# Kernel optimization log

Hardware: AMD Instinct MI355X
Metric: run time of the kernel (lower is better)

Reference implementation:

```python
import jax, jax.numpy as jnp
import numpy as np

VIEWS, N, D = 6, 20000, 512
BN_EPS = 1e-5


def setup_inputs() -> dict:
    key = jax.random.key(0)
    ks = jax.random.split(key, 8)
    s = 1.0 / np.sqrt(D)
    u = lambda k, shape: jax.random.uniform(k, shape, jnp.float32, -s, s)
    return {
        "latent_feature": jax.random.normal(ks[0], (VIEWS, N, D), jnp.float32),
        "WQ_w": u(ks[1], (D, D)), "WQ_b": u(ks[2], (D,)),
        "WK_w": u(ks[3], (D, D)), "WK_b": u(ks[4], (D,)),
        "WV_w": u(ks[5], (D, D)), "WV_b": u(ks[6], (D,)),
        "g_q": jnp.ones((D,), jnp.float32), "b_q": jnp.zeros((D,), jnp.float32),
        "g_k": jnp.ones((D,), jnp.float32), "b_k": jnp.zeros((D,), jnp.float32),
        "g_v": jnp.ones((D,), jnp.float32), "b_v": jnp.zeros((D,), jnp.float32),
    }


def _batchnorm(x, gamma, beta):
    # BatchNorm1d in training mode: stats over all (view, N) samples per channel
    mean = jnp.mean(x, axis=(0, 1), keepdims=True)
    var = jnp.mean((x - mean) ** 2, axis=(0, 1), keepdims=True)  # biased var
    return gamma * (x - mean) * jax.lax.rsqrt(var + BN_EPS) + beta


def _fro_normalize(x):
    # Frobenius norm per view over (N, D)
    n = jnp.sqrt(jnp.sum(x * x, axis=(1, 2), keepdims=True)) + 1e-8
    return x / n


def _multi_projection(P):
    dim = P.shape[0]
    P = 0.5 * (jax.nn.softmax(P, axis=0) + jax.nn.softmax(P, axis=1))
    for _ in range(10):  # fixed 10-step doubly-stochastic projection
        P1 = jnp.maximum(P, 0.0)
        P2 = P1 - (jnp.sum(P1, axis=1, keepdims=True) - 1.0) / dim
        P = P2 - (jnp.sum(P2, axis=0, keepdims=True) - 1.0) / dim
    return P


def reference(latent_feature, WQ_w, WQ_b, WK_w, WK_b, WV_w, WV_b,
              g_q, b_q, g_k, b_k, g_v, b_v):
    # latent_feature: [views, N, D]
    Q = _batchnorm(latent_feature @ WQ_w.T + WQ_b, g_q, b_q)
    K = _batchnorm(latent_feature @ WK_w.T + WK_b, g_k, b_k)
    V = _batchnorm(latent_feature @ WV_w.T + WV_b, g_v, b_v)
    Q, K, V = _fro_normalize(Q), _fro_normalize(K), _fro_normalize(V)
    P = jax.nn.sigmoid(jnp.einsum('ind,jnd->ij', Q, K))  # [views, views]
    P = _multi_projection(P)
    return jnp.einsum('ij,ind->jnd', P, V)  # [views, N, D]
```

## Files before the change

kernel.cpp:

```cpp
#include <hip/hip_runtime.h>

#define VIEWS 6
#define NPTS 20000
#define DIM 512
#define M_TOTAL (VIEWS * NPTS)

typedef __bf16 bf16_t;
typedef __attribute__((ext_vector_type(8))) __bf16 bf16x8;
typedef __attribute__((ext_vector_type(4))) float f32x4;

#define OFF_XB 0L
#define OFF_QB 122880000L
#define OFF_KB 245760000L
#define OFF_VB 368640000L
#define OFF_WB 491520000L
#define OFF_F32 493092864L
#define S_SUM 0
#define S_SSQ 9216
#define S_PPRE 18432
#define S_COEFA 18468
#define S_COEFC 20004
#define S_INVN 21540
#define S_P 21558
#define S_END 21594

__device__ __forceinline__ void gload_lds16(const void* gsrc, void* lds) {
    __builtin_amdgcn_global_load_lds(
        (const __attribute__((address_space(1))) unsigned int*)gsrc,
        (__attribute__((address_space(3))) unsigned int*)lds,
        16, 0, 0);
}

__global__ __launch_bounds__(256) void convert_bf16(
    const float* __restrict__ src, bf16_t* __restrict__ dst, long n8)
{
    long i = (long)blockIdx.x * blockDim.x + threadIdx.x;
    const long stride = (long)gridDim.x * blockDim.x;
    for (; i < n8; i += stride) {
        const float4* s = (const float4*)(src + i * 8);
        float4 x = s[0], y = s[1];
        bf16x8 o;
        o[0] = (bf16_t)x.x; o[1] = (bf16_t)x.y; o[2] = (bf16_t)x.z; o[3] = (bf16_t)x.w;
        o[4] = (bf16_t)y.x; o[5] = (bf16_t)y.y; o[6] = (bf16_t)y.z; o[7] = (bf16_t)y.w;
        *(bf16x8*)(dst + i * 8) = o;
    }
}

__global__ __launch_bounds__(256, 4) void gemm_qkv_mfma(
    const bf16_t* __restrict__ XB, const bf16_t* __restrict__ WB,
    const float* __restrict__ b0, const float* __restrict__ b1,
    const float* __restrict__ b2,
    float* __restrict__ statS, float* __restrict__ statQ,
    bf16_t* __restrict__ QB, bf16_t* __restrict__ KB, bf16_t* __restrict__ VB)
{
    const int orig = blockIdx.x;
    const int L    = (orig & 7) * 1878 + (orig >> 3);
    const int n0i  = L / 48;
    const int rem  = L - n0i * 48;
    const int v    = rem >> 3;
    const int c0   = (rem & 7) << 6;
    const int n0   = n0i * 64;
    const int nvalid = min(64, NPTS - n0);

    const int tid  = threadIdx.x;
    const int wid  = tid >> 6;
    const int lane = tid & 63;
    const int lr   = lane & 15;
    const int lk   = lane >> 4;
    const int wm   = wid >> 1;
    const int wn   = wid & 1;

    __shared__ char smem[32768];

    const bf16_t* Ag = XB + ((long)v * NPTS + n0) * DIM;

    f32x4 acc[3][2][2];
    const f32x4 zero4 = {0.f, 0.f, 0.f, 0.f};
#pragma unroll
    for (int t = 0; t < 3; ++t)
#pragma unroll
        for (int i = 0; i < 2; ++i)
#pragma unroll
            for (int j = 0; j < 2; ++j) acc[t][i][j] = zero4;

    for (int k0 = 0; k0 < DIM; k0 += 64) {
        __syncthreads();
#pragma unroll
        for (int i = 0; i < 8; ++i) {
            const int base = i * 256 + wid * 64;
            const int g    = base + lane;
            const bf16_t* src;
            if (g < 512) {
                const int row = g >> 3;
                const int kcs = (g & 7) ^ (row & 7);
                const int rowc = (row < nvalid) ? row : (nvalid - 1);
                src = Ag + (long)rowc * DIM + k0 + kcs * 8;
            } else {
                const int h   = g - 512;
                const int t   = h >> 9;
                const int idx = h & 511;
                const int row = idx >> 3;
                const int kcs = (idx & 7) ^ (row & 7);
                src = WB + ((long)t << 18) + (long)(c0 + row) * DIM + k0 + kcs * 8;
            }
            gload_lds16(src, smem + (long)base * 16);
        }
        __syncthreads();
#pragma unroll
        for (int ks = 0; ks < 2; ++ks) {
            const int kc = ks * 4 + lk;
            bf16x8 af[2];
#pragma unroll
            for (int fm = 0; fm < 2; ++fm) {
                const int rowA = wm * 32 + fm * 16 + lr;
                af[fm] = *(const bf16x8*)(smem + rowA * 128 + ((kc ^ (rowA & 7)) << 4));
            }
#pragma unroll
            for (int t = 0; t < 3; ++t) {
#pragma unroll
                for (int fn = 0; fn < 2; ++fn) {
                    const int rowB = wn * 32 + fn * 16 + lr;
                    bf16x8 bf = *(const bf16x8*)(smem + 8192 + t * 8192 +
                                                 rowB * 128 + ((kc ^ (rowB & 7)) << 4));
#pragma unroll
                    for (int fm = 0; fm < 2; ++fm)
                        acc[t][fm][fn] = __builtin_amdgcn_mfma_f32_16x16x32_bf16(
                            af[fm], bf, acc[t][fm][fn], 0, 0, 0);
                }
            }
        }
    }

    __syncthreads();
    float* redS = (float*)smem;
    float* redQ = redS + 64;
    for (int t = 0; t < 3; ++t) {
        if (tid < 128) redS[tid] = 0.f;
        __syncthreads();
        bf16_t* Obuf = (t == 0) ? QB : (t == 1) ? KB : VB;
        const float* bias = (t == 0) ? b0 : (t == 1) ? b1 : b2;
#pragma unroll
        for (int fn = 0; fn < 2; ++fn) {
            const int cl  = wn * 32 + fn * 16 + lr;
            const int col = c0 + cl;
            const float bv_ = bias[col];
            float cs = 0.f, cq = 0.f;
#pragma unroll
            for (int fm = 0; fm < 2; ++fm) {
#pragma unroll
                for (int r = 0; r < 4; ++r) {
                    const int row = wm * 32 + fm * 16 + lk * 4 + r;
                    if (row < nvalid) {
                        float val = acc[t][fm][fn][r] + bv_;
                        cs += val;
                        cq += val * val;
                        Obuf[((long)v * NPTS + n0 + row) * DIM + col] = (bf16_t)val;
                    }
                }
            }
            atomicAdd(&redS[cl], cs);
            atomicAdd(&redQ[cl], cq);
        }
        __syncthreads();
        if (tid < 64) {
            atomicAdd(&statS[(((long)t * 6 + v) << 9) + c0 + tid], redS[tid]);
            atomicAdd(&statQ[(((long)t * 6 + v) << 9) + c0 + tid], redQ[tid]);
        }
        __syncthreads();
    }
}

__global__ __launch_bounds__(512) void finalize_stats(
    const float* __restrict__ gq, const float* __restrict__ beq,
    const float* __restrict__ gk, const float* __restrict__ bek,
    const float* __restrict__ gv, const float* __restrict__ bev,
    float* __restrict__ ws2)
{
    const int t = blockIdx.x;
    const int c = threadIdx.x;
    const float* g  = (t == 0) ? gq : (t == 1) ? gk : gv;
    const float* be = (t == 0) ? beq : (t == 1) ? bek : bev;
    const float* sumbuf = ws2 + S_SUM + (long)t * 6 * 512;
    const float* ssqbuf = ws2 + S_SSQ + (long)t * 6 * 512;

    float s[6], q[6];
    float tot = 0.f, totq = 0.f;
#pragma unroll
    for (int v = 0; v < 6; ++v) {
        s[v] = sumbuf[v * 512 + c];
        q[v] = ssqbuf[v * 512 + c];
        tot += s[v]; totq += q[v];
    }
    const float invM = 1.0f / (float)M_TOTAL;
    float mean = tot * invM;
    float var  = totq * invM - mean * mean;
    float a    = g[c] * rsqrtf(var + 1e-5f);
    float cc   = be[c] - a * mean;
    ws2[S_COEFA + t * 512 + c] = a;
    ws2[S_COEFC + t * 512 + c] = cc;

    __shared__ float red[512];
    for (int v = 0; v < 6; ++v) {
        red[c] = a * a * q[v] + 2.f * a * cc * s[v] + (float)NPTS * cc * cc;
        __syncthreads();
        for (int off = 256; off > 0; off >>= 1) {
            if (c < off) red[c] += red[c + off];
            __syncthreads();
        }
        if (c == 0) ws2[S_INVN + t * 6 + v] = 1.f / (sqrtf(red[0]) + 1e-8f);
        __syncthreads();
    }
}

__global__ __launch_bounds__(256) void qk_dot(
    const bf16_t* __restrict__ QB, const bf16_t* __restrict__ KB,
    float* __restrict__ ws2)
{
    float acc[36];
#pragma unroll
    for (int c = 0; c < 36; ++c) acc[c] = 0.f;

    const float* cA = ws2 + S_COEFA;
    const long total = (long)NPTS * 64;
    for (long it = (long)blockIdx.x * 256 + threadIdx.x; it < total;
         it += (long)gridDim.x * 256) {
        const int n  = (int)(it >> 6);
        const int d8 = (int)(it & 63);

        float w8[8];
#pragma unroll
        for (int e = 0; e < 8; ++e)
            w8[e] = cA[d8 * 8 + e] * cA[512 + d8 * 8 + e];

        float qw[6][8];
#pragma unroll
        for (int i = 0; i < 6; ++i) {
            bf16x8 qv = *(const bf16x8*)(QB + ((long)i * NPTS + n) * DIM + d8 * 8);
#pragma unroll
            for (int e = 0; e < 8; ++e) qw[i][e] = (float)qv[e] * w8[e];
        }
#pragma unroll
        for (int j = 0; j < 6; ++j) {
            bf16x8 kv = *(const bf16x8*)(KB + ((long)j * NPTS + n) * DIM + d8 * 8);
            float kf[8];
#pragma unroll
            for (int e = 0; e < 8; ++e) kf[e] = (float)kv[e];
#pragma unroll
            for (int i = 0; i < 6; ++i) {
                float d = 0.f;
#pragma unroll
                for (int e = 0; e < 8; ++e) d = fmaf(qw[i][e], kf[e], d);
                acc[i * 6 + j] += d;
            }
        }
    }

    __shared__ float part[36];
    if (threadIdx.x < 36) part[threadIdx.x] = 0.f;
    __syncthreads();
    const int lane = threadIdx.x & 63;
#pragma unroll
    for (int c = 0; c < 36; ++c) {
        float x = acc[c];
#pragma unroll
        for (int m = 1; m < 64; m <<= 1) x += __shfl_xor(x, m);
        if (lane == 0) atomicAdd(&part[c], x);
    }
    __syncthreads();
    if (threadIdx.x < 36) atomicAdd(&ws2[S_PPRE + threadIdx.x], part[threadIdx.x]);
}

__global__ __launch_bounds__(512) void project_kernel(float* __restrict__ ws2)
{
    const int c = threadIdx.x;
    __shared__ float red[512];
    const float aq = ws2[S_COEFA + c],       cq = ws2[S_COEFC + c];
    const float ak = ws2[S_COEFA + 512 + c], ck = ws2[S_COEFC + 512 + c];

    float vals[13];
#pragma unroll
    for (int i = 0; i < 6; ++i) vals[i]     = aq * ck * ws2[S_SUM + i * 512 + c];
#pragma unroll
    for (int j = 0; j < 6; ++j) vals[6 + j] = cq * ak * ws2[S_SUM + (6 + j) * 512 + c];
    vals[12] = cq * ck;

    float out13[13];
#pragma unroll
    for (int r = 0; r < 13; ++r) {
        red[c] = vals[r];
        __syncthreads();
        for (int off = 256; off > 0; off >>= 1) {
            if (c < off) red[c] += red[c + off];
            __syncthreads();
        }
        out13[r] = red[0];
        __syncthreads();
    }

    if (c != 0) return;

    const float* invn = ws2 + S_INVN;
    float p[6][6];
    for (int i = 0; i < 6; ++i)
        for (int j = 0; j < 6; ++j) {
            float raw = ws2[S_PPRE + i * 6 + j] + out13[i] + out13[6 + j] +
                        (float)NPTS * out13[12];
            float z = raw * invn[i] * invn[6 + j];
            p[i][j] = 1.f / (1.f + expf(-z));
        }
    float s0[6][6], s1[6][6];
    for (int j = 0; j < 6; ++j) {
        float m = -1e30f;
        for (int i = 0; i < 6; ++i) m = fmaxf(m, p[i][j]);
        float sum = 0.f;
        for (int i = 0; i < 6; ++i) { s0[i][j] = expf(p[i][j] - m); sum += s0[i][j]; }
        for (int i = 0; i < 6; ++i) s0[i][j] /= sum;
    }
    for (int i = 0; i < 6; ++i) {
        float m = -1e30f;
        for (int j = 0; j < 6; ++j) m = fmaxf(m, p[i][j]);
        float sum = 0.f;
        for (int j = 0; j < 6; ++j) { s1[i][j] = expf(p[i][j] - m); sum += s1[i][j]; }
        for (int j = 0; j < 6; ++j) s1[i][j] /= sum;
    }
    for (int i = 0; i < 6; ++i)
        for (int j = 0; j < 6; ++j) p[i][j] = 0.5f * (s0[i][j] + s1[i][j]);

    for (int itr = 0; itr < 10; ++itr) {
        float p1[6][6];
        for (int i = 0; i < 6; ++i)
            for (int j = 0; j < 6; ++j) p1[i][j] = fmaxf(p[i][j], 0.f);
        for (int i = 0; i < 6; ++i) {
            float rs = 0.f;
            for (int j = 0; j < 6; ++j) rs += p1[i][j];
            float adj = (rs - 1.f) * (1.f / 6.f);
            for (int j = 0; j < 6; ++j) p1[i][j] -= adj;
        }
        for (int j = 0; j < 6; ++j) {
            float cs = 0.f;
            for (int i = 0; i < 6; ++i) cs += p1[i][j];
            float adj = (cs - 1.f) * (1.f / 6.f);
            for (int i = 0; i < 6; ++i) p1[i][j] -= adj;
        }
        for (int i = 0; i < 6; ++i)
            for (int j = 0; j < 6; ++j) p[i][j] = p1[i][j];
    }
    for (int i = 0; i < 6; ++i)
        for (int j = 0; j < 6; ++j) ws2[S_P + i * 6 + j] = p[i][j];
}

__global__ __launch_bounds__(256) void combine_out(
    const bf16_t* __restrict__ VB, const float* __restrict__ ws2,
    float* __restrict__ out)
{
    float w[36];
#pragma unroll
    for (int c = 0; c < 36; ++c)
        w[c] = ws2[S_P + c] * ws2[S_INVN + 12 + c / 6];
    const float* av = ws2 + S_COEFA + 1024;
    const float* cv = ws2 + S_COEFC + 1024;

    const long total = (long)NPTS * 64;
    for (long it = (long)blockIdx.x * 256 + threadIdx.x; it < total;
         it += (long)gridDim.x * 256) {
        const int n  = (int)(it >> 6);
        const int d8 = (int)(it & 63);
        float a8[8], c8[8];
#pragma unroll
        for (int e = 0; e < 8; ++e) { a8[e] = av[d8 * 8 + e]; c8[e] = cv[d8 * 8 + e]; }

        float o[6][8];
#pragma unroll
        for (int j = 0; j < 6; ++j)
#pragma unroll
            for (int e = 0; e < 8; ++e) o[j][e] = 0.f;

#pragma unroll
        for (int i = 0; i < 6; ++i) {
            bf16x8 xv = *(const bf16x8*)(VB + ((long)i * NPTS + n) * DIM + d8 * 8);
            float vn[8];
#pragma unroll
            for (int e = 0; e < 8; ++e) vn[e] = fmaf(a8[e], (float)xv[e], c8[e]);
#pragma unroll
            for (int j = 0; j < 6; ++j) {
                const float wi = w[i * 6 + j];
#pragma unroll
                for (int e = 0; e < 8; ++e) o[j][e] = fmaf(wi, vn[e], o[j][e]);
            }
        }
#pragma unroll
        for (int j = 0; j < 6; ++j) {
            float* dst = out + ((long)j * NPTS + n) * DIM + d8 * 8;
            *(float4*)dst       = *(const float4*)&o[j][0];
            *(float4*)(dst + 4) = *(const float4*)&o[j][4];
        }
    }
}

extern "C" void kernel_launch(void* const* d_in, const int* in_sizes, int n_in,
                              void* d_out, int out_size, void* d_ws, size_t ws_size,
                              hipStream_t stream)
{
    const float* X   = (const float*)d_in[0];
    const float* Wq  = (const float*)d_in[1];
    const float* bq  = (const float*)d_in[2];
    const float* Wk  = (const float*)d_in[3];
    const float* bk  = (const float*)d_in[4];
    const float* Wv  = (const float*)d_in[5];
    const float* bv  = (const float*)d_in[6];
    const float* gq  = (const float*)d_in[7];
    const float* beq = (const float*)d_in[8];
    const float* gk  = (const float*)d_in[9];
    const float* bek = (const float*)d_in[10];
    const float* gv  = (const float*)d_in[11];
    const float* bev = (const float*)d_in[12];

    char* w = (char*)d_ws;
    bf16_t* XB = (bf16_t*)(w + OFF_XB);
    bf16_t* QB = (bf16_t*)(w + OFF_QB);
    bf16_t* KB = (bf16_t*)(w + OFF_KB);
    bf16_t* VB = (bf16_t*)(w + OFF_VB);
    bf16_t* WB = (bf16_t*)(w + OFF_WB);
    float* ws2 = (float*)(w + OFF_F32);
    float* out = (float*)d_out;

    hipMemsetAsync(ws2, 0, S_END * sizeof(float), stream);

    convert_bf16<<<2048, 256, 0, stream>>>(X, XB, (long)M_TOTAL * DIM / 8);
    convert_bf16<<<128, 256, 0, stream>>>(Wq, WB,           (long)DIM * DIM / 8);
    convert_bf16<<<128, 256, 0, stream>>>(Wk, WB + 262144,  (long)DIM * DIM / 8);
    convert_bf16<<<128, 256, 0, stream>>>(Wv, WB + 524288,  (long)DIM * DIM / 8);

    gemm_qkv_mfma<<<15024, 256, 0, stream>>>(XB, WB, bq, bk, bv,
                                             ws2 + S_SUM, ws2 + S_SSQ, QB, KB, VB);
    finalize_stats<<<3, 512, 0, stream>>>(gq, beq, gk, bek, gv, bev, ws2);
    qk_dot<<<2048, 256, 0, stream>>>(QB, KB, ws2);
    project_kernel<<<1, 512, 0, stream>>>(ws2);
    combine_out<<<2048, 256, 0, stream>>>(VB, ws2, out);
}
```

Measured before the change: 1.113 ms.

## Enlarge QKV GEMM row tile to 256 and merge bf16 conversion launches

The QKV GEMM block tile grows from 64 to 256 rows, with each of four waves computing 64 rows by 64 columns for all three projections. Shared memory rises to 56 KB, accumulators to 48 fragments, and launch bounds drop to 2 blocks per CU. This reuses each loaded weight tile across four times as many rows, cutting redundant weight loads and the number of blocks. The four fp32-to-bf16 conversion launches are also merged into one kernel. The cost is higher register pressure and lower occupancy.

```diff
diff --git a/kernel.cpp b/kernel.cpp
--- a/kernel.cpp
+++ b/kernel.cpp
@@ -31,22 +31,37 @@
         16, 0, 0);
 }
 
-__global__ __launch_bounds__(256) void convert_bf16(
-    const float* __restrict__ src, bf16_t* __restrict__ dst, long n8)
-{
-    long i = (long)blockIdx.x * blockDim.x + threadIdx.x;
-    const long stride = (long)gridDim.x * blockDim.x;
-    for (; i < n8; i += stride) {
-        const float4* s = (const float4*)(src + i * 8);
-        float4 x = s[0], y = s[1];
+__global__ __launch_bounds__(256) void convert_all(
+    const float* __restrict__ X,
+    const float* __restrict__ Wq, const float* __restrict__ Wk,
+    const float* __restrict__ Wv,
+    bf16_t* __restrict__ XB, bf16_t* __restrict__ WB)
+{
+    const long NX = (long)M_TOTAL * DIM / 8;
+    const long NW = (long)DIM * DIM / 8;
+    const long total = NX + 3 * NW;
+    for (long i = (long)blockIdx.x * 256 + threadIdx.x; i < total;
+         i += (long)gridDim.x * 256) {
+        const float* s;
+        bf16_t* d;
+        if (i < NX) { s = X + i * 8; d = XB + i * 8; }
+        else {
+            long w = i - NX;
+            int t = (int)(w / NW);
+            long r = w - (long)t * NW;
+            const float* W = (t == 0) ? Wq : (t == 1) ? Wk : Wv;
+            s = W + r * 8;
+            d = WB + w * 8;
+        }
+        float4 x = ((const float4*)s)[0], y = ((const float4*)s)[1];
         bf16x8 o;
         o[0] = (bf16_t)x.x; o[1] = (bf16_t)x.y; o[2] = (bf16_t)x.z; o[3] = (bf16_t)x.w;
         o[4] = (bf16_t)y.x; o[5] = (bf16_t)y.y; o[6] = (bf16_t)y.z; o[7] = (bf16_t)y.w;
-        *(bf16x8*)(dst + i * 8) = o;
-    }
-}
-
-__global__ __launch_bounds__(256, 4) void gemm_qkv_mfma(
+        *(bf16x8*)d = o;
+    }
+}
+
+__global__ __launch_bounds__(256, 2) void gemm_qkv_mfma(
     const bf16_t* __restrict__ XB, const bf16_t* __restrict__ WB,
     const float* __restrict__ b0, const float* __restrict__ b1,
     const float* __restrict__ b2,
@@ -54,49 +69,47 @@
     bf16_t* __restrict__ QB, bf16_t* __restrict__ KB, bf16_t* __restrict__ VB)
 {
     const int orig = blockIdx.x;
-    const int L    = (orig & 7) * 1878 + (orig >> 3);
+    const int L    = (orig & 7) * 474 + (orig >> 3);
     const int n0i  = L / 48;
     const int rem  = L - n0i * 48;
     const int v    = rem >> 3;
     const int c0   = (rem & 7) << 6;
-    const int n0   = n0i * 64;
-    const int nvalid = min(64, NPTS - n0);
+    const int n0   = n0i * 256;
+    const int nvalid = min(256, NPTS - n0);
 
     const int tid  = threadIdx.x;
     const int wid  = tid >> 6;
     const int lane = tid & 63;
     const int lr   = lane & 15;
     const int lk   = lane >> 4;
-    const int wm   = wid >> 1;
-    const int wn   = wid & 1;
-
-    __shared__ char smem[32768];
+
+    __shared__ char smem[57344];
 
     const bf16_t* Ag = XB + ((long)v * NPTS + n0) * DIM;
 
-    f32x4 acc[3][2][2];
+    f32x4 acc[3][4][4];
     const f32x4 zero4 = {0.f, 0.f, 0.f, 0.f};
 #pragma unroll
     for (int t = 0; t < 3; ++t)
 #pragma unroll
-        for (int i = 0; i < 2; ++i)
-#pragma unroll
-            for (int j = 0; j < 2; ++j) acc[t][i][j] = zero4;
+        for (int i = 0; i < 4; ++i)
+#pragma unroll
+            for (int j = 0; j < 4; ++j) acc[t][i][j] = zero4;
 
     for (int k0 = 0; k0 < DIM; k0 += 64) {
         __syncthreads();
 #pragma unroll
-        for (int i = 0; i < 8; ++i) {
+        for (int i = 0; i < 14; ++i) {
             const int base = i * 256 + wid * 64;
             const int g    = base + lane;
             const bf16_t* src;
-            if (g < 512) {
+            if (g < 2048) {
                 const int row = g >> 3;
                 const int kcs = (g & 7) ^ (row & 7);
                 const int rowc = (row < nvalid) ? row : (nvalid - 1);
                 src = Ag + (long)rowc * DIM + k0 + kcs * 8;
             } else {
-                const int h   = g - 512;
+                const int h   = g - 2048;
                 const int t   = h >> 9;
                 const int idx = h & 511;
                 const int row = idx >> 3;
@@ -109,21 +122,21 @@
 #pragma unroll
         for (int ks = 0; ks < 2; ++ks) {
             const int kc = ks * 4 + lk;
-            bf16x8 af[2];
-#pragma unroll
-            for (int fm = 0; fm < 2; ++fm) {
-                const int rowA = wm * 32 + fm * 16 + lr;
+            bf16x8 af[4];
+#pragma unroll
+            for (int fm = 0; fm < 4; ++fm) {
+                const int rowA = wid * 64 + fm * 16 + lr;
                 af[fm] = *(const bf16x8*)(smem + rowA * 128 + ((kc ^ (rowA & 7)) << 4));
             }
 #pragma unroll
             for (int t = 0; t < 3; ++t) {
 #pragma unroll
-                for (int fn = 0; fn < 2; ++fn) {
-                    const int rowB = wn * 32 + fn * 16 + lr;
-                    bf16x8 bf = *(const bf16x8*)(smem + 8192 + t * 8192 +
+                for (int fn = 0; fn < 4; ++fn) {
+                    const int rowB = fn * 16 + lr;
+                    bf16x8 bf = *(const bf16x8*)(smem + 32768 + t * 8192 +
                                                  rowB * 128 + ((kc ^ (rowB & 7)) << 4));
 #pragma unroll
-                    for (int fm = 0; fm < 2; ++fm)
+                    for (int fm = 0; fm < 4; ++fm)
                         acc[t][fm][fn] = __builtin_amdgcn_mfma_f32_16x16x32_bf16(
                             af[fm], bf, acc[t][fm][fn], 0, 0, 0);
                 }
@@ -140,16 +153,16 @@
         bf16_t* Obuf = (t == 0) ? QB : (t == 1) ? KB : VB;
         const float* bias = (t == 0) ? b0 : (t == 1) ? b1 : b2;
 #pragma unroll
-        for (int fn = 0; fn < 2; ++fn) {
-            const int cl  = wn * 32 + fn * 16 + lr;
+        for (int fn = 0; fn < 4; ++fn) {
+            const int cl  = fn * 16 + lr;
             const int col = c0 + cl;
             const float bv_ = bias[col];
             float cs = 0.f, cq = 0.f;
 #pragma unroll
-            for (int fm = 0; fm < 2; ++fm) {
+            for (int fm = 0; fm < 4; ++fm) {
 #pragma unroll
                 for (int r = 0; r < 4; ++r) {
-                    const int row = wm * 32 + fm * 16 + lk * 4 + r;
+                    const int row = wid * 64 + fm * 16 + lk * 4 + r;
                     if (row < nvalid) {
                         float val = acc[t][fm][fn][r] + bv_;
                         cs += val;
@@ -426,13 +439,10 @@
 
     hipMemsetAsync(ws2, 0, S_END * sizeof(float), stream);
 
-    convert_bf16<<<2048, 256, 0, stream>>>(X, XB, (long)M_TOTAL * DIM / 8);
-    convert_bf16<<<128, 256, 0, stream>>>(Wq, WB,           (long)DIM * DIM / 8);
-    convert_bf16<<<128, 256, 0, stream>>>(Wk, WB + 262144,  (long)DIM * DIM / 8);
-    convert_bf16<<<128, 256, 0, stream>>>(Wv, WB + 524288,  (long)DIM * DIM / 8);
-
-    gemm_qkv_mfma<<<15024, 256, 0, stream>>>(XB, WB, bq, bk, bv,
-                                             ws2 + S_SUM, ws2 + S_SSQ, QB, KB, VB);
+    convert_all<<<2048, 256, 0, stream>>>(X, Wq, Wk, Wv, XB, WB);
+
+    gemm_qkv_mfma<<<3792, 256, 0, stream>>>(XB, WB, bq, bk, bv,
+                                            ws2 + S_SUM, ws2 + S_SSQ, QB, KB, VB);
     finalize_stats<<<3, 512, 0, stream>>>(gq, beq, gk, bek, gv, bev, ws2);
     qk_dot<<<2048, 256, 0, stream>>>(QB, KB, ws2);
     project_kernel<<<1, 512, 0, stream>>>(ws2);
```

Result: faster. 1.042 ms (-6.4%).
